# Kernel tuning notes

Hardware: AMD Instinct MI355X
Metric: run time of the kernel (lower is better)

Reference implementation:

```python
import jax, jax.numpy as jnp
import numpy as np

# Model dims (from module defaults / chosen plant dims)
B, T = 1024, 1024
NY, NX, NW, NU = 32, 16, 128, 8   # input(obs), state, nonlin, output(action)
DT = 0.01
N_ITER_COLD = 30   # torchdeq f_max_iter
N_ITER_WARM = 5    # solver_kwargs f_max_iter when reusing warm start
LOG_STD_INIT = -1.6094379124341003


def setup_inputs() -> dict:
    key = jax.random.key(0)
    ks = jax.random.split(key, 11)
    s = 0.1  # keep the implicit/recurrent dynamics stable over 1024 RK4 steps
    obs = jax.random.normal(ks[0], (B, T, NY), jnp.float32)
    x0 = jnp.zeros((B, NX), jnp.float32)
    A_T = (-0.5 * jnp.eye(NX) + 0.05 * jax.random.normal(ks[1], (NX, NX))).astype(jnp.float32)
    Bw_T = s * jax.random.normal(ks[2], (NW, NX), jnp.float32)
    By_T = s * jax.random.normal(ks[3], (NY, NX), jnp.float32)
    Cv_T = s * jax.random.normal(ks[4], (NX, NW), jnp.float32)
    Dvw_T = 0.05 * jax.random.normal(ks[5], (NW, NW), jnp.float32)  # small -> fixed-point contraction
    Dvy_T = s * jax.random.normal(ks[6], (NY, NW), jnp.float32)
    Cu_T = s * jax.random.normal(ks[7], (NX, NU), jnp.float32)
    Duw_T = s * jax.random.normal(ks[8], (NW, NU), jnp.float32)
    Duy_T = s * jax.random.normal(ks[9], (NY, NU), jnp.float32)
    log_stds = LOG_STD_INIT * jnp.ones((NU,), jnp.float32)
    return dict(obs=obs, x0=x0, A_T=A_T, Bw_T=Bw_T, By_T=By_T, Cv_T=Cv_T,
                Dvw_T=Dvw_T, Dvy_T=Dvy_T, Cu_T=Cu_T, Duw_T=Duw_T, Duy_T=Duy_T,
                log_stds=log_stds)


def reference(obs, x0, A_T, Bw_T, By_T, Cv_T, Dvw_T, Dvy_T, Cu_T, Duw_T, Duy_T, log_stds):
    def fp_solve(w0, bias, n_iter):
        # w = tanh(x@Cv_T + w@Dvw_T + y@Dvy_T); bias = x@Cv_T + y@Dvy_T precomputed
        def body(i, w):
            return jnp.tanh(bias + w @ Dvw_T)
        return jax.lax.fori_loop(0, n_iter, body, w0)

    def xdot(x, w, y):
        return x @ A_T + w @ Bw_T + y @ By_T

    def step(x, y, w_guess, n_w):
        y_bias = y @ Dvy_T  # [B, NW], reused across RK stages
        wk = fp_solve(w_guess, x @ Cv_T + y_bias, n_w)
        k1 = xdot(x, wk, y)
        def stage(xs, w_prev):
            ws = fp_solve(w_prev, xs @ Cv_T + y_bias, N_ITER_WARM)
            return xdot(xs, ws, y), ws
        k2, w2 = stage(x + 0.5 * DT * k1, wk)
        k3, w3 = stage(x + 0.5 * DT * k2, w2)
        k4, w4 = stage(x + DT * k3, w3)
        x_next = x + (DT / 6.0) * (k1 + 2.0 * k2 + 2.0 * k3 + k4)
        u = x @ Cu_T + wk @ Duw_T + y @ Duy_T  # action from current state/nonlin/obs
        return x_next, w4, u

    # First timestep: cold DEQ solve (30 iters), no warm start
    w0 = jnp.zeros((x0.shape[0], NW), x0.dtype)
    x1, wg, u0 = step(x0, obs[:, 0], w0, N_ITER_COLD)

    # Remaining timesteps: warm-started solves (5 iters), sequential via scan
    def scan_body(carry, y_t):
        x, wg = carry
        x_next, w_next, u = step(x, y_t, wg, N_ITER_WARM)
        return (x_next, w_next), u
    obs_rest = jnp.swapaxes(obs[:, 1:], 0, 1)  # [T-1, B, NY]
    _, us = jax.lax.scan(scan_body, (x1, wg), obs_rest)

    actions = jnp.concatenate([u0[:, None, :], jnp.swapaxes(us, 0, 1)], axis=1)  # [B, T, NU]
    outputs = jnp.concatenate(
        [actions, jnp.broadcast_to(log_stds, actions.shape)], axis=-1)  # [B, T, 2*NU]
    return outputs
```

## Files before the change

kernel.cpp:

```cpp
#include <hip/hip_runtime.h>
#include <hip/hip_bf16.h>


#define T_SZ 1024
#define NY 32
#define NX 16
#define NW 128
#define NU 8
#define DT_F 0.01f
#define NCOLD 30
#define NWARM 5

typedef __attribute__((ext_vector_type(8))) short bf8v;
typedef __attribute__((ext_vector_type(4))) float f4v;

#define MFMA16(a, b, c) __builtin_amdgcn_mfma_f32_16x16x32_bf16((a), (b), (c), 0, 0, 0)

__device__ __forceinline__ unsigned short f2bf(float f) {
  return __builtin_bit_cast(unsigned short, __float2bfloat16(f));
}
__device__ __forceinline__ float bf2f(unsigned short u) {
  return __bfloat162float(__builtin_bit_cast(__hip_bfloat16, u));
}
__device__ __forceinline__ float tanh_fast(float z) {
  float e = __builtin_amdgcn_exp2f(z * 2.8853900817779268f);
  return 1.0f - 2.0f * __builtin_amdgcn_rcpf(e + 1.0f);
}

__global__ __launch_bounds__(256, 1) void rinn_kernel(
    const float* __restrict__ obs, const float* __restrict__ x0,
    const float* __restrict__ A_T, const float* __restrict__ Bw_T,
    const float* __restrict__ By_T, const float* __restrict__ Cv_T,
    const float* __restrict__ Dvw_T, const float* __restrict__ Dvy_T,
    const float* __restrict__ Cu_T, const float* __restrict__ Duw_T,
    const float* __restrict__ Duy_T, const float* __restrict__ log_stds,
    float* __restrict__ out) {
  __shared__ __align__(16) char wlds[8192];
  __shared__ __align__(16) char xlds[2048];

  const int tid = (int)threadIdx.x;
  const int wv = tid >> 6;
  const int lane = tid & 63;
  const int r = lane & 15;
  const int h = lane >> 4;
  const long grow = (long)(blockIdx.x * 16 + r);
  const int sw = (r & 7) << 4;

  bf8v Adw[2][4], Ady[2], Acv[2];
#pragma unroll
  for (int gi = 0; gi < 2; ++gi) {
    const int j = 16 * (2 * wv + gi) + r;
#pragma unroll
    for (int f = 0; f < 4; ++f)
#pragma unroll
      for (int q = 0; q < 8; ++q)
        Adw[gi][f][q] = (short)f2bf(Dvw_T[(32 * f + 8 * h + q) * NW + j]);
#pragma unroll
    for (int q = 0; q < 8; ++q) {
      Ady[gi][q] = (short)f2bf(Dvy_T[(8 * h + q) * NW + j]);
      Acv[gi][q] = (short)f2bf(Cv_T[((8 * h + q) & 15) * NW + j]);
    }
  }
  bf8v Ax16, Ak[4], Ay32;
  {
    const bool is0 = (wv == 0), is1 = (wv == 1);
#pragma unroll
    for (int q = 0; q < 8; ++q) {
      int k = 8 * h + q;
      float vx = 0.f, vy = 0.f;
      if (is0)              { vx = A_T[(k & 15) * NX + r];  vy = By_T[k * NX + r]; }
      else if (is1 && r < NU){ vx = Cu_T[(k & 15) * NU + r]; vy = Duy_T[k * NU + r]; }
      Ax16[q] = (short)f2bf(vx);
      Ay32[q] = (short)f2bf(vy);
    }
#pragma unroll
    for (int f = 0; f < 4; ++f)
#pragma unroll
      for (int q = 0; q < 8; ++q) {
        int k = 32 * f + 8 * h + q;
        float v = 0.f;
        if (is0)               v = Bw_T[k * NX + r];
        else if (is1 && r < NU) v = Duw_T[k * NU + r];
        Ak[f][q] = (short)f2bf(v);
      }
  }
  f4v lsv;
#pragma unroll
  for (int i = 0; i < 4; ++i) lsv[i] = (h >= 2) ? log_stds[4 * (h - 2) + i] : 0.f;

  f4v xr = {0.f, 0.f, 0.f, 0.f};
  if (wv == 0) {
#pragma unroll
    for (int i = 0; i < 4; ++i) xr[i] = x0[grow * NX + 4 * h + i];
  }

  auto write_x = [&](int buf, f4v v) {
    unsigned short b0 = f2bf(v[0]), b1 = f2bf(v[1]), b2 = f2bf(v[2]), b3 = f2bf(v[3]);
    uint2 hp, lp;
    hp.x = (unsigned)b0 | ((unsigned)b1 << 16);
    hp.y = (unsigned)b2 | ((unsigned)b3 << 16);
    lp.x = (unsigned)f2bf(v[0] - bf2f(b0)) | ((unsigned)f2bf(v[1] - bf2f(b1)) << 16);
    lp.y = (unsigned)f2bf(v[2] - bf2f(b2)) | ((unsigned)f2bf(v[3] - bf2f(b3)) << 16);
    char* base = xlds + buf * 1024 + r * 64;
    *(uint2*)(base + 8 * h) = hp;
    *(uint2*)(base + 32 + 8 * h) = lp;
  };

  {
    uint4 z; z.x = z.y = z.z = z.w = 0u;
    ((uint4*)wlds)[tid] = z;
    if (wv == 0) write_x(0, xr);
  }
  __syncthreads();

  const float* orow = obs + grow * T_SZ * NY;
  bf8v By0, By1;
  {
    float yf[8];
#pragma unroll
    for (int q = 0; q < 8; ++q) yf[q] = orow[8 * h + q];
#pragma unroll
    for (int q = 0; q < 8; ++q) {
      unsigned short hi = f2bf(yf[q]);
      By0[q] = (short)hi;
      By1[q] = (short)f2bf(yf[q] - bf2f(hi));
    }
  }

  int cur = 0;
  f4v cb[2], cbias[2];

  auto do_solve = [&](int n) {
    for (int it = 0; it < n; ++it) {
      bf8v bw[4];
#pragma unroll
      for (int f = 0; f < 4; ++f)
        bw[f] = *(const bf8v*)(wlds + cur * 4096 + r * 256 + ((64 * f + 16 * h) ^ sw));
#pragma unroll
      for (int gi = 0; gi < 2; ++gi) {
        f4v c = cbias[gi];
#pragma unroll
        for (int f = 0; f < 4; ++f) c = MFMA16(Adw[gi][f], bw[f], c);
        uint2 pk;
        pk.x = (unsigned)f2bf(tanh_fast(c[0])) | ((unsigned)f2bf(tanh_fast(c[1])) << 16);
        pk.y = (unsigned)f2bf(tanh_fast(c[2])) | ((unsigned)f2bf(tanh_fast(c[3])) << 16);
        *(uint2*)(wlds + (cur ^ 1) * 4096 + r * 256 + ((32 * (2 * wv + gi) + 8 * h) ^ sw)) = pk;
      }
      __syncthreads();
      cur ^= 1;
    }
  };

  auto stage_bias = [&](int xbuf) {
    bf8v bx = *(const bf8v*)(xlds + xbuf * 1024 + r * 64 + 16 * h);
#pragma unroll
    for (int gi = 0; gi < 2; ++gi) cbias[gi] = MFMA16(Acv[gi], bx, cb[gi]);
  };

  auto kchain = [&](int xbuf) -> f4v {
    bf8v bw[4];
#pragma unroll
    for (int f = 0; f < 4; ++f)
      bw[f] = *(const bf8v*)(wlds + cur * 4096 + r * 256 + ((64 * f + 16 * h) ^ sw));
    bf8v bx = *(const bf8v*)(xlds + xbuf * 1024 + r * 64 + 16 * h);
    f4v c = {0.f, 0.f, 0.f, 0.f};
    c = MFMA16(Ax16, bx, c);
#pragma unroll
    for (int f = 0; f < 4; ++f) c = MFMA16(Ak[f], bw[f], c);
    c = MFMA16(Ay32, By0, c);
    c = MFMA16(Ay32, By1, c);
    return c;
  };

  f4v acc = {0.f, 0.f, 0.f, 0.f};
  for (int t = 0; t < T_SZ; ++t) {
#pragma unroll
    for (int gi = 0; gi < 2; ++gi) {
      f4v c = {0.f, 0.f, 0.f, 0.f};
      c = MFMA16(Ady[gi], By0, c);
      c = MFMA16(Ady[gi], By1, c);
      cb[gi] = c;
    }
    float yn[8];
    {
      const long tn = (t + 1 < T_SZ) ? (t + 1) : t;
#pragma unroll
      for (int q = 0; q < 8; ++q) yn[q] = orow[tn * NY + 8 * h + q];
    }

    stage_bias(0);
    do_solve(t == 0 ? NCOLD : NWARM);
    f4v kv = {0.f, 0.f, 0.f, 0.f};
    if (wv < 2) kv = kchain(0);
    if (wv == 1) {
      f4v sv;
#pragma unroll
      for (int i = 0; i < 4; ++i) sv[i] = (h < 2) ? kv[i] : lsv[i];
      *(f4v*)(out + (grow * T_SZ + t) * 16 + 4 * h) = sv;
    }
    f4v xs;
    if (wv == 0) {
      acc = kv;
#pragma unroll
      for (int i = 0; i < 4; ++i) xs[i] = xr[i] + (0.5f * DT_F) * kv[i];
      write_x(1, xs);
    }
    __syncthreads();

    stage_bias(1);
    do_solve(NWARM);
    if (wv == 0) {
      kv = kchain(1);
#pragma unroll
      for (int i = 0; i < 4; ++i) { acc[i] += 2.f * kv[i]; xs[i] = xr[i] + (0.5f * DT_F) * kv[i]; }
      write_x(0, xs);
    }
    __syncthreads();

    stage_bias(0);
    do_solve(NWARM);
    if (wv == 0) {
      kv = kchain(0);
#pragma unroll
      for (int i = 0; i < 4; ++i) { acc[i] += 2.f * kv[i]; xs[i] = xr[i] + DT_F * kv[i]; }
      write_x(1, xs);
    }
    __syncthreads();

    stage_bias(1);
    do_solve(NWARM);
    if (wv == 0) {
      kv = kchain(1);
#pragma unroll
      for (int i = 0; i < 4; ++i) xr[i] += (DT_F / 6.f) * (acc[i] + kv[i]);
      write_x(0, xr);
    }
#pragma unroll
    for (int q = 0; q < 8; ++q) {
      unsigned short hi = f2bf(yn[q]);
      By0[q] = (short)hi;
      By1[q] = (short)f2bf(yn[q] - bf2f(hi));
    }
    __syncthreads();
  }
}

extern "C" void kernel_launch(void* const* d_in, const int* in_sizes, int n_in,
                              void* d_out, int out_size, void* d_ws, size_t ws_size,
                              hipStream_t stream) {
  (void)in_sizes; (void)n_in; (void)out_size; (void)d_ws; (void)ws_size;
  rinn_kernel<<<64, 256, 0, stream>>>(
      (const float*)d_in[0], (const float*)d_in[1], (const float*)d_in[2],
      (const float*)d_in[3], (const float*)d_in[4], (const float*)d_in[5],
      (const float*)d_in[6], (const float*)d_in[7], (const float*)d_in[8],
      (const float*)d_in[9], (const float*)d_in[10], (const float*)d_in[11],
      (float*)d_out);
}
```

Before: 7.224 ms.

## Replicate state update per wave to drop RK stage barriers and fold tanh scale

Every wave now computes the xdot chain redundantly and keeps its own private copy of x in LDS. This removes the four per-timestep __syncthreads that waited on wave 0's state update. The tanh 2·log2(e) scale is folded into the bf16 weight matrices. The weight-row permutation lets each wave reuse its freshly computed w slice from registers instead of reading it back from LDS, saving one LDS read per iteration. In exchange every wave issues extra MFMAs for the state chain, and pre-scaling the weights before bf16 rounding changes rounding slightly.

```diff
diff --git a/kernel.cpp b/kernel.cpp
--- a/kernel.cpp
+++ b/kernel.cpp
@@ -10,6 +10,7 @@
 #define DT_F 0.01f
 #define NCOLD 30
 #define NWARM 5
+#define KAPPA 2.8853900817779268f
 
 typedef __attribute__((ext_vector_type(8))) short bf8v;
 typedef __attribute__((ext_vector_type(4))) float f4v;
@@ -22,9 +23,10 @@
 __device__ __forceinline__ float bf2f(unsigned short u) {
   return __bfloat162float(__builtin_bit_cast(__hip_bfloat16, u));
 }
-__device__ __forceinline__ float tanh_fast(float z) {
-  float e = __builtin_amdgcn_exp2f(z * 2.8853900817779268f);
-  return 1.0f - 2.0f * __builtin_amdgcn_rcpf(e + 1.0f);
+__device__ __forceinline__ short tanh_bf(float z) {
+  float e = __builtin_amdgcn_exp2f(z);
+  float r = __builtin_amdgcn_rcpf(e + 1.0f);
+  return (short)f2bf(1.0f - 2.0f * r);
 }
 
 __global__ __launch_bounds__(256, 1) void rinn_kernel(
@@ -36,7 +38,7 @@
     const float* __restrict__ Duy_T, const float* __restrict__ log_stds,
     float* __restrict__ out) {
   __shared__ __align__(16) char wlds[8192];
-  __shared__ __align__(16) char xlds[2048];
+  __shared__ __align__(16) char xlds[4096];
 
   const int tid = (int)threadIdx.x;
   const int wv = tid >> 6;
@@ -45,71 +47,78 @@
   const int h = lane >> 4;
   const long grow = (long)(blockIdx.x * 16 + r);
   const int sw = (r & 7) << 4;
-
-  bf8v Adw[2][4], Ady[2], Acv[2];
+  const int rbase = r * 256;
+
+  const int ro0 = (64 * wv + 16 * h) ^ sw;
+  const int ro1 = (64 * ((wv + 1) & 3) + 16 * h) ^ sw;
+  const int ro2 = (64 * ((wv + 2) & 3) + 16 * h) ^ sw;
+  const int ro3 = (64 * ((wv + 3) & 3) + 16 * h) ^ sw;
+
+  bf8v Adw[2][4], Acv[2], Ady[2];
 #pragma unroll
   for (int gi = 0; gi < 2; ++gi) {
-    const int j = 16 * (2 * wv + gi) + r;
-#pragma unroll
-    for (int f = 0; f < 4; ++f)
+    const int j = 32 * wv + 8 * (r >> 2) + 4 * gi + (r & 3);
+#pragma unroll
+    for (int s = 0; s < 4; ++s) {
+      const int f = (wv + s) & 3;
 #pragma unroll
       for (int q = 0; q < 8; ++q)
-        Adw[gi][f][q] = (short)f2bf(Dvw_T[(32 * f + 8 * h + q) * NW + j]);
-#pragma unroll
-    for (int q = 0; q < 8; ++q) {
-      Ady[gi][q] = (short)f2bf(Dvy_T[(8 * h + q) * NW + j]);
-      Acv[gi][q] = (short)f2bf(Cv_T[((8 * h + q) & 15) * NW + j]);
-    }
-  }
-  bf8v Ax16, Ak[4], Ay32;
-  {
-    const bool is0 = (wv == 0), is1 = (wv == 1);
-#pragma unroll
-    for (int q = 0; q < 8; ++q) {
-      int k = 8 * h + q;
-      float vx = 0.f, vy = 0.f;
-      if (is0)              { vx = A_T[(k & 15) * NX + r];  vy = By_T[k * NX + r]; }
-      else if (is1 && r < NU){ vx = Cu_T[(k & 15) * NU + r]; vy = Duy_T[k * NU + r]; }
-      Ax16[q] = (short)f2bf(vx);
-      Ay32[q] = (short)f2bf(vy);
-    }
-#pragma unroll
-    for (int f = 0; f < 4; ++f)
-#pragma unroll
-      for (int q = 0; q < 8; ++q) {
-        int k = 32 * f + 8 * h + q;
-        float v = 0.f;
-        if (is0)               v = Bw_T[k * NX + r];
-        else if (is1 && r < NU) v = Duw_T[k * NU + r];
-        Ak[f][q] = (short)f2bf(v);
-      }
+        Adw[gi][s][q] = (short)f2bf(KAPPA * Dvw_T[(32 * f + 8 * h + q) * NW + j]);
+    }
+#pragma unroll
+    for (int q = 0; q < 8; ++q) {
+      Acv[gi][q] = (short)f2bf(KAPPA * Cv_T[((8 * h + q) & 15) * NW + j]);
+      Ady[gi][q] = (short)f2bf(KAPPA * Dvy_T[(8 * h + q) * NW + j]);
+    }
+  }
+  bf8v Ax, Akx[4], Ayx, Au, Aku[4], Ayu;
+#pragma unroll
+  for (int q = 0; q < 8; ++q) {
+    int k = 8 * h + q;
+    Ax[q] = (short)f2bf(A_T[(k & 15) * NX + r]);
+    Ayx[q] = (short)f2bf(By_T[k * NX + r]);
+    float cu = 0.f, dy = 0.f;
+    if (wv == 1 && r < NU) { cu = Cu_T[(k & 15) * NU + r]; dy = Duy_T[k * NU + r]; }
+    Au[q] = (short)f2bf(cu);
+    Ayu[q] = (short)f2bf(dy);
+  }
+#pragma unroll
+  for (int s = 0; s < 4; ++s) {
+    const int f = (wv + s) & 3;
+#pragma unroll
+    for (int q = 0; q < 8; ++q) {
+      int k = 32 * f + 8 * h + q;
+      Akx[s][q] = (short)f2bf(Bw_T[k * NX + r]);
+      float du = 0.f;
+      if (wv == 1 && r < NU) du = Duw_T[k * NU + r];
+      Aku[s][q] = (short)f2bf(du);
+    }
   }
   f4v lsv;
 #pragma unroll
   for (int i = 0; i < 4; ++i) lsv[i] = (h >= 2) ? log_stds[4 * (h - 2) + i] : 0.f;
 
-  f4v xr = {0.f, 0.f, 0.f, 0.f};
-  if (wv == 0) {
-#pragma unroll
-    for (int i = 0; i < 4; ++i) xr[i] = x0[grow * NX + 4 * h + i];
-  }
-
-  auto write_x = [&](int buf, f4v v) {
+  f4v xr;
+#pragma unroll
+  for (int i = 0; i < 4; ++i) xr[i] = x0[grow * NX + 4 * h + i];
+
+  char* xbase = xlds + wv * 1024;
+  auto write_x = [&](f4v v) {
     unsigned short b0 = f2bf(v[0]), b1 = f2bf(v[1]), b2 = f2bf(v[2]), b3 = f2bf(v[3]);
     uint2 hp, lp;
     hp.x = (unsigned)b0 | ((unsigned)b1 << 16);
     hp.y = (unsigned)b2 | ((unsigned)b3 << 16);
     lp.x = (unsigned)f2bf(v[0] - bf2f(b0)) | ((unsigned)f2bf(v[1] - bf2f(b1)) << 16);
     lp.y = (unsigned)f2bf(v[2] - bf2f(b2)) | ((unsigned)f2bf(v[3] - bf2f(b3)) << 16);
-    char* base = xlds + buf * 1024 + r * 64;
-    *(uint2*)(base + 8 * h) = hp;
-    *(uint2*)(base + 32 + 8 * h) = lp;
+    *(uint2*)(xbase + r * 64 + 8 * h) = hp;
+    *(uint2*)(xbase + r * 64 + 32 + 8 * h) = lp;
   };
+  auto read_bx = [&]() { return *(const bf8v*)(xbase + r * 64 + 16 * h); };
 
   {
     uint4 z; z.x = z.y = z.z = z.w = 0u;
     ((uint4*)wlds)[tid] = z;
-    if (wv == 0) write_x(0, xr);
+    write_x(xr);
   }
   __syncthreads();
 
@@ -127,121 +136,103 @@
     }
   }
 
-  int cur = 0;
-  f4v cb[2], cbias[2];
-
-  auto do_solve = [&](int n) {
-    for (int it = 0; it < n; ++it) {
-      bf8v bw[4];
-#pragma unroll
-      for (int f = 0; f < 4; ++f)
-        bw[f] = *(const bf8v*)(wlds + cur * 4096 + r * 256 + ((64 * f + 16 * h) ^ sw));
-#pragma unroll
-      for (int gi = 0; gi < 2; ++gi) {
-        f4v c = cbias[gi];
-#pragma unroll
-        for (int f = 0; f < 4; ++f) c = MFMA16(Adw[gi][f], bw[f], c);
-        uint2 pk;
-        pk.x = (unsigned)f2bf(tanh_fast(c[0])) | ((unsigned)f2bf(tanh_fast(c[1])) << 16);
-        pk.y = (unsigned)f2bf(tanh_fast(c[2])) | ((unsigned)f2bf(tanh_fast(c[3])) << 16);
-        *(uint2*)(wlds + (cur ^ 1) * 4096 + r * 256 + ((32 * (2 * wv + gi) + 8 * h) ^ sw)) = pk;
-      }
-      __syncthreads();
-      cur ^= 1;
-    }
+  int co = 0;
+  bf8v of8 = {};
+  f4v cbias0, cbias1;
+
+  auto solve_iter = [&]() {
+    const char* wb = wlds + co;
+    bf8v b1 = *(const bf8v*)(wb + rbase + ro1);
+    bf8v b2 = *(const bf8v*)(wb + rbase + ro2);
+    bf8v b3 = *(const bf8v*)(wb + rbase + ro3);
+    f4v c0 = MFMA16(Adw[0][0], of8, cbias0);
+    f4v c1 = MFMA16(Adw[1][0], of8, cbias1);
+    c0 = MFMA16(Adw[0][1], b1, c0);  c1 = MFMA16(Adw[1][1], b1, c1);
+    c0 = MFMA16(Adw[0][2], b2, c0);  c1 = MFMA16(Adw[1][2], b2, c1);
+    c0 = MFMA16(Adw[0][3], b3, c0);  c1 = MFMA16(Adw[1][3], b3, c1);
+    bf8v o;
+    o[0] = tanh_bf(c0[0]); o[1] = tanh_bf(c0[1]); o[2] = tanh_bf(c0[2]); o[3] = tanh_bf(c0[3]);
+    o[4] = tanh_bf(c1[0]); o[5] = tanh_bf(c1[1]); o[6] = tanh_bf(c1[2]); o[7] = tanh_bf(c1[3]);
+    of8 = o;
+    *(bf8v*)(wlds + (co ^ 4096) + rbase + ro0) = o;
+    __syncthreads();
+    co ^= 4096;
   };
 
-  auto stage_bias = [&](int xbuf) {
-    bf8v bx = *(const bf8v*)(xlds + xbuf * 1024 + r * 64 + 16 * h);
-#pragma unroll
-    for (int gi = 0; gi < 2; ++gi) cbias[gi] = MFMA16(Acv[gi], bx, cb[gi]);
-  };
-
-  auto kchain = [&](int xbuf) -> f4v {
-    bf8v bw[4];
-#pragma unroll
-    for (int f = 0; f < 4; ++f)
-      bw[f] = *(const bf8v*)(wlds + cur * 4096 + r * 256 + ((64 * f + 16 * h) ^ sw));
-    bf8v bx = *(const bf8v*)(xlds + xbuf * 1024 + r * 64 + 16 * h);
-    f4v c = {0.f, 0.f, 0.f, 0.f};
-    c = MFMA16(Ax16, bx, c);
-#pragma unroll
-    for (int f = 0; f < 4; ++f) c = MFMA16(Ak[f], bw[f], c);
-    c = MFMA16(Ay32, By0, c);
-    c = MFMA16(Ay32, By1, c);
+  auto kchain = [&](bf8v bx, int t, bool do_u) -> f4v {
+    const char* wb = wlds + co;
+    bf8v b1 = *(const bf8v*)(wb + rbase + ro1);
+    bf8v b2 = *(const bf8v*)(wb + rbase + ro2);
+    bf8v b3 = *(const bf8v*)(wb + rbase + ro3);
+    f4v z = {0.f, 0.f, 0.f, 0.f};
+    f4v c = MFMA16(Ax, bx, z);
+    c = MFMA16(Akx[0], of8, c);
+    c = MFMA16(Akx[1], b1, c); c = MFMA16(Akx[2], b2, c); c = MFMA16(Akx[3], b3, c);
+    c = MFMA16(Ayx, By0, c);   c = MFMA16(Ayx, By1, c);
+    if (do_u && wv == 1) {
+      f4v cu = MFMA16(Au, bx, z);
+      cu = MFMA16(Aku[0], of8, cu);
+      cu = MFMA16(Aku[1], b1, cu); cu = MFMA16(Aku[2], b2, cu); cu = MFMA16(Aku[3], b3, cu);
+      cu = MFMA16(Ayu, By0, cu);   cu = MFMA16(Ayu, By1, cu);
+      f4v sv;
+#pragma unroll
+      for (int i = 0; i < 4; ++i) sv[i] = (h < 2) ? cu[i] : lsv[i];
+      *(f4v*)(out + (grow * T_SZ + t) * 16 + 4 * h) = sv;
+    }
     return c;
   };
 
-  f4v acc = {0.f, 0.f, 0.f, 0.f};
   for (int t = 0; t < T_SZ; ++t) {
-#pragma unroll
-    for (int gi = 0; gi < 2; ++gi) {
-      f4v c = {0.f, 0.f, 0.f, 0.f};
-      c = MFMA16(Ady[gi], By0, c);
-      c = MFMA16(Ady[gi], By1, c);
-      cb[gi] = c;
-    }
+    f4v zz = {0.f, 0.f, 0.f, 0.f};
+    f4v cb0 = MFMA16(Ady[0], By0, zz); cb0 = MFMA16(Ady[0], By1, cb0);
+    f4v cb1 = MFMA16(Ady[1], By0, zz); cb1 = MFMA16(Ady[1], By1, cb1);
+
+    bf8v bx = read_bx();
+    cbias0 = MFMA16(Acv[0], bx, cb0); cbias1 = MFMA16(Acv[1], bx, cb1);
+    const int n1 = (t == 0) ? NCOLD : NWARM;
+    for (int it = 0; it < n1; ++it) solve_iter();
     float yn[8];
     {
       const long tn = (t + 1 < T_SZ) ? (t + 1) : t;
 #pragma unroll
       for (int q = 0; q < 8; ++q) yn[q] = orow[tn * NY + 8 * h + q];
     }
-
-    stage_bias(0);
-    do_solve(t == 0 ? NCOLD : NWARM);
-    f4v kv = {0.f, 0.f, 0.f, 0.f};
-    if (wv < 2) kv = kchain(0);
-    if (wv == 1) {
-      f4v sv;
-#pragma unroll
-      for (int i = 0; i < 4; ++i) sv[i] = (h < 2) ? kv[i] : lsv[i];
-      *(f4v*)(out + (grow * T_SZ + t) * 16 + 4 * h) = sv;
-    }
-    f4v xs;
-    if (wv == 0) {
-      acc = kv;
-#pragma unroll
-      for (int i = 0; i < 4; ++i) xs[i] = xr[i] + (0.5f * DT_F) * kv[i];
-      write_x(1, xs);
-    }
-    __syncthreads();
-
-    stage_bias(1);
-    do_solve(NWARM);
-    if (wv == 0) {
-      kv = kchain(1);
-#pragma unroll
-      for (int i = 0; i < 4; ++i) { acc[i] += 2.f * kv[i]; xs[i] = xr[i] + (0.5f * DT_F) * kv[i]; }
-      write_x(0, xs);
-    }
-    __syncthreads();
-
-    stage_bias(0);
-    do_solve(NWARM);
-    if (wv == 0) {
-      kv = kchain(0);
-#pragma unroll
-      for (int i = 0; i < 4; ++i) { acc[i] += 2.f * kv[i]; xs[i] = xr[i] + DT_F * kv[i]; }
-      write_x(1, xs);
-    }
-    __syncthreads();
-
-    stage_bias(1);
-    do_solve(NWARM);
-    if (wv == 0) {
-      kv = kchain(1);
-#pragma unroll
-      for (int i = 0; i < 4; ++i) xr[i] += (DT_F / 6.f) * (acc[i] + kv[i]);
-      write_x(0, xr);
-    }
+    f4v kv = kchain(bx, t, true);
+    f4v acc = kv, xs;
+#pragma unroll
+    for (int i = 0; i < 4; ++i) xs[i] = xr[i] + (0.5f * DT_F) * kv[i];
+    write_x(xs);
+
+    bx = read_bx();
+    cbias0 = MFMA16(Acv[0], bx, cb0); cbias1 = MFMA16(Acv[1], bx, cb1);
+    for (int it = 0; it < NWARM; ++it) solve_iter();
+    kv = kchain(bx, t, false);
+#pragma unroll
+    for (int i = 0; i < 4; ++i) { acc[i] += 2.f * kv[i]; xs[i] = xr[i] + (0.5f * DT_F) * kv[i]; }
+    write_x(xs);
+
+    bx = read_bx();
+    cbias0 = MFMA16(Acv[0], bx, cb0); cbias1 = MFMA16(Acv[1], bx, cb1);
+    for (int it = 0; it < NWARM; ++it) solve_iter();
+    kv = kchain(bx, t, false);
+#pragma unroll
+    for (int i = 0; i < 4; ++i) { acc[i] += 2.f * kv[i]; xs[i] = xr[i] + DT_F * kv[i]; }
+    write_x(xs);
+
+    bx = read_bx();
+    cbias0 = MFMA16(Acv[0], bx, cb0); cbias1 = MFMA16(Acv[1], bx, cb1);
+    for (int it = 0; it < NWARM; ++it) solve_iter();
+    kv = kchain(bx, t, false);
+#pragma unroll
+    for (int i = 0; i < 4; ++i) xr[i] += (DT_F / 6.f) * (acc[i] + kv[i]);
+    write_x(xr);
+
 #pragma unroll
     for (int q = 0; q < 8; ++q) {
       unsigned short hi = f2bf(yn[q]);
       By0[q] = (short)hi;
       By1[q] = (short)f2bf(yn[q] - bf2f(hi));
     }
-    __syncthreads();
   }
 }
 
```

New measurement: 6.200 ms. 1.17x faster.
